# Performance work log

Hardware: AMD Instinct MI355X
Metric: run time of the kernel (lower is better)

The kernel has to match this reference:

```python
import jax, jax.numpy as jnp
import numpy as np

L2_REG = 0.02


def setup_inputs() -> dict:
    key = jax.random.key(0)
    k1, k2 = jax.random.split(key)
    n, d = 4096, 1024
    anchors = jax.random.normal(k1, (n, d), dtype=jnp.float32)
    positives = jax.random.normal(k2, (n, d), dtype=jnp.float32)
    return {"anchors": anchors, "positives": positives}


def reference(anchors, positives):
    # Fused equivalent of the per-row masked_select loop:
    # x[i, j] = a_i . (p_j - p_i) = S[i, j] - S[i, i], for j != i
    n = anchors.shape[0]
    S = anchors @ positives.T                     # (n, n)
    x = S - jnp.diag(S)[:, None]                  # subtract anchor-positive sim per row
    offdiag = ~jnp.eye(n, dtype=bool)
    # sum over negatives j != i of exp(x[i, j])
    s = jnp.sum(jnp.where(offdiag, jnp.exp(x), 0.0), axis=1)  # (n,)
    n_pair = jnp.mean(jnp.log1p(s))
    l2 = jnp.sum(anchors ** 2 + positives ** 2) / n
    return n_pair + L2_REG * l2
```

## Files before the change

kernel.cpp:

```cpp
#include <hip/hip_runtime.h>
#include <math.h>
#include <stdint.h>

#define N 4096
#define Dm 1024
#define BM 128
#define BN 128
#define BK 64
#define NCB (N / 64)

typedef __attribute__((ext_vector_type(8))) short bf16x8;
typedef __attribute__((ext_vector_type(4))) float f32x4;

typedef const void __attribute__((address_space(1)))* gas_t;
typedef void __attribute__((address_space(3)))* las_t;

static __device__ __forceinline__ void gload_lds16(const void* g, void* l) {
    __builtin_amdgcn_global_load_lds((gas_t)g, (las_t)l, 16, 0, 0);
}

static __device__ __forceinline__ unsigned short f2bf(float f) {
    unsigned int u = __float_as_uint(f);
    unsigned int r = (u + 0x7fff + ((u >> 16) & 1)) >> 16;
    return (unsigned short)r;
}

__global__ __launch_bounds__(256) void prep_kernel(const float* __restrict__ A,
                                                   const float* __restrict__ P,
                                                   unsigned short* __restrict__ Abf,
                                                   unsigned short* __restrict__ Pbf,
                                                   float* __restrict__ D,
                                                   float* __restrict__ rowl2) {
    int t = threadIdx.x;
    int lane = t & 63;
    int row = blockIdx.x * 4 + (t >> 6);
    const float4* a4 = (const float4*)(A + (size_t)row * Dm);
    const float4* p4 = (const float4*)(P + (size_t)row * Dm);
    ushort4* ao = (ushort4*)(Abf + (size_t)row * Dm);
    ushort4* po = (ushort4*)(Pbf + (size_t)row * Dm);
    float dot = 0.0f, l2 = 0.0f;
#pragma unroll
    for (int c = 0; c < 4; ++c) {
        int idx = c * 64 + lane;
        float4 a = a4[idx], p = p4[idx];
        ushort4 ab, pb;
        ab.x = f2bf(a.x); ab.y = f2bf(a.y); ab.z = f2bf(a.z); ab.w = f2bf(a.w);
        pb.x = f2bf(p.x); pb.y = f2bf(p.y); pb.z = f2bf(p.z); pb.w = f2bf(p.w);
        ao[idx] = ab; po[idx] = pb;
        dot += a.x * p.x + a.y * p.y + a.z * p.z + a.w * p.w;
        l2  += a.x * a.x + a.y * a.y + a.z * a.z + a.w * a.w
             + p.x * p.x + p.y * p.y + p.z * p.z + p.w * p.w;
    }
#pragma unroll
    for (int off = 32; off; off >>= 1) {
        dot += __shfl_xor(dot, off, 64);
        l2  += __shfl_xor(l2,  off, 64);
    }
    if (lane == 0) {
        D[row]     = dot;
        rowl2[row] = l2;
    }
}

__global__ __launch_bounds__(256) void npair_mfma(const unsigned short* __restrict__ Abf,
                                                  const unsigned short* __restrict__ Pbf,
                                                  const float* __restrict__ D,
                                                  float* __restrict__ Mpart,
                                                  float* __restrict__ Spart) {
    __shared__ unsigned short At[BM * BK];
    __shared__ unsigned short Bt[BN * BK];
    __shared__ float Ds[BM];
    int tid = threadIdx.x;
    int wid = tid >> 6, lane = tid & 63;
    int wr = wid >> 1, wc = wid & 1;
    int row0 = blockIdx.y * BM, col0 = blockIdx.x * BN;

    const unsigned short* gA[4]; const unsigned short* gB[4];
    unsigned short* lA[4]; unsigned short* lB[4];
#pragma unroll
    for (int b = 0; b < 4; ++b) {
        int L = b * 256 + tid;
        int row = L >> 3, c = L & 7;
        int kch = c ^ (row & 7);
        gA[b] = Abf + (size_t)(row0 + row) * Dm + (kch << 3);
        gB[b] = Pbf + (size_t)(col0 + row) * Dm + (kch << 3);
        lA[b] = At + (size_t)L * 8;
        lB[b] = Bt + (size_t)L * 8;
    }
    if (tid < BM) Ds[tid] = D[row0 + tid];

    f32x4 acc[4][4] = {};

    for (int kt = 0; kt < Dm; kt += BK) {
        __syncthreads();
#pragma unroll
        for (int b = 0; b < 4; ++b) {
            gload_lds16(gA[b] + kt, lA[b]);
            gload_lds16(gB[b] + kt, lB[b]);
        }
        __syncthreads();
#pragma unroll
        for (int ks = 0; ks < 2; ++ks) {
            bf16x8 af[4], bfr[4];
#pragma unroll
            for (int i = 0; i < 4; ++i) {
                int g = (ks << 2) + (lane >> 4);
                int arow = wr * 64 + i * 16 + (lane & 15);
                af[i]  = *(const bf16x8*)(At + arow * BK + ((g ^ (arow & 7)) << 3));
                int brow = wc * 64 + i * 16 + (lane & 15);
                bfr[i] = *(const bf16x8*)(Bt + brow * BK + ((g ^ (brow & 7)) << 3));
            }
#pragma unroll
            for (int i = 0; i < 4; ++i)
#pragma unroll
                for (int j = 0; j < 4; ++j)
                    acc[i][j] = __builtin_amdgcn_mfma_f32_16x16x32_bf16(af[i], bfr[j], acc[i][j], 0, 0, 0);
        }
    }

    int cb = blockIdx.x * 2 + wc;
#pragma unroll
    for (int rt = 0; rt < 4; ++rt) {
        int rloc = wr * 64 + rt * 16 + ((lane >> 4) << 2);
#pragma unroll
        for (int e = 0; e < 4; ++e) {
            int gr = row0 + rloc + e;
            float Dv = Ds[rloc + e];
            float xs[4];
            float m = -INFINITY;
#pragma unroll
            for (int ct = 0; ct < 4; ++ct) {
                int gc = col0 + wc * 64 + ct * 16 + (lane & 15);
                float x = acc[rt][ct][e] - Dv;
                if (gr == gc) x = -INFINITY;
                xs[ct] = x;
                m = fmaxf(m, x);
            }
#pragma unroll
            for (int off = 8; off; off >>= 1) m = fmaxf(m, __shfl_xor(m, off, 64));
            float s = 0.0f;
#pragma unroll
            for (int ct = 0; ct < 4; ++ct) s += __expf(xs[ct] - m);
#pragma unroll
            for (int off = 8; off; off >>= 1) s += __shfl_xor(s, off, 64);
            if ((lane & 15) == 0) {
                Mpart[(size_t)gr * NCB + cb] = m;
                Spart[(size_t)gr * NCB + cb] = s;
            }
        }
    }
}

__global__ __launch_bounds__(256) void combine_rows(const float* __restrict__ Mpart,
                                                    const float* __restrict__ Spart,
                                                    float* __restrict__ loss) {
    int t = threadIdx.x;
    int lane = t & 63;
    int w = t >> 6;
#pragma unroll
    for (int r = 0; r < 2; ++r) {
        int row = blockIdx.x * 8 + w * 2 + r;
        float mp = Mpart[(size_t)row * NCB + lane];
        float sp = Spart[(size_t)row * NCB + lane];
        float m = mp;
#pragma unroll
        for (int off = 32; off; off >>= 1) m = fmaxf(m, __shfl_xor(m, off, 64));
        float s = sp * __expf(mp - m);
#pragma unroll
        for (int off = 32; off; off >>= 1) s += __shfl_xor(s, off, 64);
        if (lane == 0) loss[row] = m + logf(__expf(-m) + s);
    }
}

__global__ __launch_bounds__(256) void final_reduce(const float* __restrict__ loss,
                                                    const float* __restrict__ rowl2,
                                                    float* __restrict__ out) {
    int t = threadIdx.x;
    float accL = 0.0f, acc2 = 0.0f;
    for (int i = t; i < N; i += 256) {
        accL += loss[i];
        acc2 += rowl2[i];
    }
#pragma unroll
    for (int off = 32; off; off >>= 1) {
        accL += __shfl_xor(accL, off, 64);
        acc2 += __shfl_xor(acc2, off, 64);
    }
    __shared__ float sa[4], sb[4];
    int wave = t >> 6;
    if ((t & 63) == 0) { sa[wave] = accL; sb[wave] = acc2; }
    __syncthreads();
    if (t == 0) {
        float L  = sa[0] + sa[1] + sa[2] + sa[3];
        float l2 = sb[0] + sb[1] + sb[2] + sb[3];
        out[0] = L / (float)N + 0.02f * (l2 / (float)N);
    }
}

extern "C" void kernel_launch(void* const* d_in, const int* in_sizes, int n_in,
                              void* d_out, int out_size, void* d_ws, size_t ws_size,
                              hipStream_t stream) {
    const float* A = (const float*)d_in[0];
    const float* P = (const float*)d_in[1];
    float* out = (float*)d_out;

    unsigned short* Abf = (unsigned short*)d_ws;
    unsigned short* Pbf = Abf + (size_t)N * Dm;
    float* D     = (float*)(Pbf + (size_t)N * Dm);
    float* rowl2 = D + N;
    float* loss  = rowl2 + N;
    float* Mpart = loss + N;
    float* Spart = Mpart + (size_t)N * NCB;

    prep_kernel<<<N / 4, 256, 0, stream>>>(A, P, Abf, Pbf, D, rowl2);
    dim3 grid(N / BN, N / BM);
    npair_mfma<<<grid, 256, 0, stream>>>(Abf, Pbf, D, Mpart, Spart);
    combine_rows<<<N / 8, 256, 0, stream>>>(Mpart, Spart, loss);
    final_reduce<<<1, 256, 0, stream>>>(loss, rowl2, out);
}
```

Baseline: 131.7 us.

## Remap GEMM tiles per XCD for L2 locality and pre-reduce row losses per block

The GEMM kernel remaps linear block IDs so that each of the 8 XCDs gets a contiguous 16x8 patch of output tiles. The aim is for blocks sharing an L2 to reuse the same A and P rows. Separately, combine_rows now sums its 8 row losses and row L2 values into per-block partials, so final_reduce reads 512 partials instead of looping over 4096 entries twice. The remap assumes a round-robin dispatch of blocks to XCDs and a 32x32 grid.

```diff
diff --git a/kernel.cpp b/kernel.cpp
--- a/kernel.cpp
+++ b/kernel.cpp
@@ -8,6 +8,7 @@
 #define BN 128
 #define BK 64
 #define NCB (N / 64)
+#define NPART 512
 
 typedef __attribute__((ext_vector_type(8))) short bf16x8;
 typedef __attribute__((ext_vector_type(4))) float f32x4;
@@ -73,7 +74,12 @@
     int tid = threadIdx.x;
     int wid = tid >> 6, lane = tid & 63;
     int wr = wid >> 1, wc = wid & 1;
-    int row0 = blockIdx.y * BM, col0 = blockIdx.x * BN;
+
+    int bid = blockIdx.y * gridDim.x + blockIdx.x;
+    int xcd = bid & 7, lid = bid >> 3;
+    int by = (xcd >> 2) * 16 + (lid >> 3);
+    int bx = (xcd & 3) * 8 + (lid & 7);
+    int row0 = by * BM, col0 = bx * BN;
 
     const unsigned short* gA[4]; const unsigned short* gB[4];
     unsigned short* lA[4]; unsigned short* lB[4];
@@ -118,7 +124,7 @@
         }
     }
 
-    int cb = blockIdx.x * 2 + wc;
+    int cb = bx * 2 + wc;
 #pragma unroll
     for (int rt = 0; rt < 4; ++rt) {
         int rloc = wr * 64 + rt * 16 + ((lane >> 4) << 2);
@@ -153,10 +159,13 @@
 
 __global__ __launch_bounds__(256) void combine_rows(const float* __restrict__ Mpart,
                                                     const float* __restrict__ Spart,
-                                                    float* __restrict__ loss) {
+                                                    const float* __restrict__ rowl2,
+                                                    float* __restrict__ partL,
+                                                    float* __restrict__ partR) {
     int t = threadIdx.x;
     int lane = t & 63;
     int w = t >> 6;
+    __shared__ float ls[8];
 #pragma unroll
     for (int r = 0; r < 2; ++r) {
         int row = blockIdx.x * 8 + w * 2 + r;
@@ -168,19 +177,25 @@
         float s = sp * __expf(mp - m);
 #pragma unroll
         for (int off = 32; off; off >>= 1) s += __shfl_xor(s, off, 64);
-        if (lane == 0) loss[row] = m + logf(__expf(-m) + s);
-    }
-}
-
-__global__ __launch_bounds__(256) void final_reduce(const float* __restrict__ loss,
-                                                    const float* __restrict__ rowl2,
+        if (lane == 0) ls[w * 2 + r] = m + logf(__expf(-m) + s);
+    }
+    __syncthreads();
+    if (t == 0) {
+        int r8 = blockIdx.x * 8;
+        float L = 0.0f, R = 0.0f;
+#pragma unroll
+        for (int r = 0; r < 8; ++r) { L += ls[r]; R += rowl2[r8 + r]; }
+        partL[blockIdx.x] = L;
+        partR[blockIdx.x] = R;
+    }
+}
+
+__global__ __launch_bounds__(256) void final_reduce(const float* __restrict__ partL,
+                                                    const float* __restrict__ partR,
                                                     float* __restrict__ out) {
     int t = threadIdx.x;
-    float accL = 0.0f, acc2 = 0.0f;
-    for (int i = t; i < N; i += 256) {
-        accL += loss[i];
-        acc2 += rowl2[i];
-    }
+    float accL = partL[t] + partL[t + 256];
+    float acc2 = partR[t] + partR[t + 256];
 #pragma unroll
     for (int off = 32; off; off >>= 1) {
         accL += __shfl_xor(accL, off, 64);
@@ -208,13 +223,14 @@
     unsigned short* Pbf = Abf + (size_t)N * Dm;
     float* D     = (float*)(Pbf + (size_t)N * Dm);
     float* rowl2 = D + N;
-    float* loss  = rowl2 + N;
-    float* Mpart = loss + N;
+    float* partL = rowl2 + N;
+    float* partR = partL + NPART;
+    float* Mpart = partR + NPART;
     float* Spart = Mpart + (size_t)N * NCB;
 
     prep_kernel<<<N / 4, 256, 0, stream>>>(A, P, Abf, Pbf, D, rowl2);
     dim3 grid(N / BN, N / BM);
     npair_mfma<<<grid, 256, 0, stream>>>(Abf, Pbf, D, Mpart, Spart);
-    combine_rows<<<N / 8, 256, 0, stream>>>(Mpart, Spart, loss);
-    final_reduce<<<1, 256, 0, stream>>>(loss, rowl2, out);
-}
+    combine_rows<<<N / 8, 256, 0, stream>>>(Mpart, Spart, rowl2, partL, partR);
+    final_reduce<<<1, 256, 0, stream>>>(partL, partR, out);
+}
```

After: 125.0 us. 5.1% less time.
